# Optimization experiments

Measured on AMD Instinct MI355X. Metric: run time of the kernel, lower is better.

The kernel has to match this reference:

```python
import jax, jax.numpy as jnp
import numpy as np
from jax import lax

B, N, T, E = 16, 2048, 48, 32
C0, C1 = 64, 64
H1, H2 = 256, 128
NPRED = 12
KT = 3
SCALE = float(np.sqrt(C1))


def setup_inputs() -> dict:
    key = jax.random.key(0)
    ks = jax.random.split(key, 20)
    def lin(k, fin, fout):
        bound = 1.0 / np.sqrt(fin)
        kw, kb = jax.random.split(k)
        W = jax.random.uniform(kw, (fin, fout), jnp.float32, -bound, bound)
        b = jax.random.uniform(kb, (fout,), jnp.float32, -bound, bound)
        return W, b
    x = jax.random.normal(ks[0], (B, N, T, E), jnp.float32)
    W_in, b_in = lin(ks[1], E, C0)
    # conv kernel laid out WIO for lax.conv_general_dilated ('NWC','WIO','NWC')
    bound = 1.0 / np.sqrt(C0 * KT)
    W_conv = jax.random.uniform(ks[2], (KT, C0, C1), jnp.float32, -bound, bound)
    b_conv = jax.random.uniform(ks[3], (C1,), jnp.float32, -bound, bound)
    Wq, bq = lin(ks[4], C1, C1)
    Wk, bk = lin(ks[5], C1, C1)
    Wv, bv = lin(ks[6], C1, C1)
    W1, b1 = lin(ks[7], C1, H1)
    W2, b2 = lin(ks[8], H1, H2)
    W3, b3 = lin(ks[9], H2, NPRED)
    return dict(x=x, W_in=W_in, b_in=b_in, W_conv=W_conv, b_conv=b_conv,
                Wq=Wq, bq=bq, Wk=Wk, bk=bk, Wv=Wv, bv=bv,
                W1=W1, b1=b1, W2=W2, b2=b2, W3=W3, b3=b3)


def reference(x, W_in, b_in, W_conv, b_conv, Wq, bq, Wk, bk, Wv, bv,
              W1, b1, W2, b2, W3, b3):
    Bs, Ns, Ts, Es = x.shape
    # input linear, fold nodes into batch (weights shared across nodes)
    h = jnp.einsum('bnte,ec->bntc', x, W_in) + b_in          # [B,N,T,C0]
    h = h.reshape(Bs * Ns, Ts, C0)                            # [BN,T,C0]
    # temporal conv over T, kernel KT, pad 1 each side (matches Conv2d (Kt,1), pad (1,0))
    h = lax.conv_general_dilated(h, W_conv, window_strides=(1,),
                                 padding=[(1, 1)],
                                 dimension_numbers=('NWC', 'WIO', 'NWC')) + b_conv
    h = jax.nn.relu(h)                                        # [BN,T,C1]
    q = h @ Wq + bq
    k = h @ Wk + bk
    v = h @ Wv + bv
    scores = jnp.einsum('btd,bsd->bts', q, k) / SCALE         # [BN,T,T]
    attn = jax.nn.softmax(scores, axis=-1)
    ctx = jnp.einsum('bts,bsd->btd', attn, v)                 # [BN,T,C1]
    last = ctx[:, -1, :]                                      # [BN,C1]
    # output MLP (dropout is identity in eval/reference)
    z = jax.nn.relu(last @ W1 + b1)
    z = jax.nn.relu(z @ W2 + b2)
    pred = z @ W3 + b3                                        # [BN,NPRED]
    out = pred.reshape(Bs, Ns, NPRED)                         # [B,N,P]
    out = jnp.transpose(out, (0, 2, 1))[:, None]              # [B,1,P,N]
    return out
```

## Files before the change

### kernel.cpp

```cpp
#include <hip/hip_runtime.h>
#include <hip/hip_bf16.h>
#include <math.h>

#define TT 48
#define NSEQ (16*2048)
#define NP 12

typedef __bf16 bf16x8 __attribute__((ext_vector_type(8)));
typedef float  f32x4  __attribute__((ext_vector_type(4)));

#define OFF_WCC 0
#define OFF_WK  6144
#define OFF_WV  10240
#define OFF_WQ  14336
#define OFF_W1  18432
#define OFF_W2  34816
#define WS_BTOT 33792
#define WS_BC0  33856
#define WS_BC2  33920
#define WS_CTX  33984

__device__ __forceinline__ f32x4 zero4() {
  f32x4 z; z[0] = 0.f; z[1] = 0.f; z[2] = 0.f; z[3] = 0.f; return z;
}

union PackU { bf16x8 v; __hip_bfloat162 h[4]; };

__device__ __forceinline__ bf16x8 pack8(float4 a, float4 b) {
  PackU u;
  u.h[0] = __float22bfloat162_rn(make_float2(a.x, a.y));
  u.h[1] = __float22bfloat162_rn(make_float2(a.z, a.w));
  u.h[2] = __float22bfloat162_rn(make_float2(b.x, b.y));
  u.h[3] = __float22bfloat162_rn(make_float2(b.z, b.w));
  return u.v;
}

__global__ __launch_bounds__(256) void prep_kernel(
    const float* __restrict__ W_in, const float* __restrict__ b_in,
    const float* __restrict__ W_conv, const float* __restrict__ b_conv,
    const float* __restrict__ Wk, const float* __restrict__ Wv,
    const float* __restrict__ Wq, const float* __restrict__ W1,
    const float* __restrict__ W2, float* __restrict__ ws)
{
  __bf16* wsb = (__bf16*)ws;
  const int tid = threadIdx.x;
  const int bid = blockIdx.x;
  if (bid < 24) {
    int gid = bid * 256 + tid;
    int kk = gid >> 6;
    int c  = gid & 63;
    int dt = kk >> 5;
    int e  = kk & 31;
    const float* wrow = W_in + e * 64;
    const float* wc   = W_conv + dt * 4096 + c;
    float acc = 0.f;
    #pragma unroll 8
    for (int c0 = 0; c0 < 64; ++c0)
      acc = fmaf(wrow[c0], wc[c0 * 64], acc);
    wsb[OFF_WCC + ((kk >> 3) * 64 + c) * 8 + (kk & 7)] = (__bf16)acc;
  } else if (bid < 40) {
    int gid = (bid - 24) * 256 + tid;
    int kk = gid >> 6, c = gid & 63;
    wsb[OFF_WK + ((kk >> 3) * 64 + c) * 8 + (kk & 7)] = (__bf16)Wk[kk * 64 + c];
  } else if (bid < 56) {
    int gid = (bid - 40) * 256 + tid;
    int kk = gid >> 6, c = gid & 63;
    wsb[OFF_WV + ((kk >> 3) * 64 + c) * 8 + (kk & 7)] = (__bf16)Wv[kk * 64 + c];
  } else if (bid < 72) {
    int gid = (bid - 56) * 256 + tid;
    int kk = gid >> 6, c = gid & 63;
    wsb[OFF_WQ + ((kk >> 3) * 64 + c) * 8 + (kk & 7)] = (__bf16)Wq[kk * 64 + c];
  } else if (bid < 136) {
    int gid = (bid - 72) * 256 + tid;
    int kk = gid >> 8, n = gid & 255;
    wsb[OFF_W1 + ((kk >> 3) * 256 + n) * 8 + (kk & 7)] = (__bf16)W1[kk * 256 + n];
  } else if (bid < 264) {
    int gid = (bid - 136) * 256 + tid;
    int kk = gid >> 7, n = gid & 127;
    wsb[OFF_W2 + ((kk >> 3) * 128 + n) * 8 + (kk & 7)] = (__bf16)W2[kk * 128 + n];
  } else if (tid < 64) {
    int c = tid;
    float s[3];
    for (int dt = 0; dt < 3; ++dt) {
      const float* wc = W_conv + dt * 4096 + c;
      float a = 0.f;
      for (int c0 = 0; c0 < 64; ++c0) a = fmaf(b_in[c0], wc[c0 * 64], a);
      s[dt] = a;
    }
    ws[WS_BC0 + c]  = s[0];
    ws[WS_BC2 + c]  = s[2];
    ws[WS_BTOT + c] = s[0] + s[1] + s[2] + b_conv[c];
  }
}

__global__ __launch_bounds__(128, 4) void attn_kernel(
    const float* __restrict__ x,
    const float* __restrict__ bq, const float* __restrict__ bk,
    const float* __restrict__ bv,
    const float* __restrict__ ws, float* __restrict__ ctx)
{
  __shared__ __bf16 h1s[2][48 * 66];

  const int tid  = threadIdx.x;
  const int lane = tid & 63;
  const int wv   = tid >> 6;
  const int m16  = lane & 15;
  const int quad = lane >> 4;
  const int seq  = blockIdx.x * 2 + wv;
  __bf16* h1 = h1s[wv];

  const __bf16* wsb  = (const __bf16*)ws;
  const bf16x8* WccB = (const bf16x8*)(wsb + OFF_WCC);
  const bf16x8* WkB  = (const bf16x8*)(wsb + OFF_WK);
  const bf16x8* WvB  = (const bf16x8*)(wsb + OFF_WV);
  const bf16x8* WqB  = (const bf16x8*)(wsb + OFF_WQ);
  const float*  wsf  = ws;
  const float*  xseq = x + (size_t)seq * (TT * 32);

  bf16x8 af[3][3];
  #pragma unroll
  for (int mt = 0; mt < 3; ++mt)
    #pragma unroll
    for (int ks = 0; ks < 3; ++ks) {
      const int tg = mt * 16 + m16 + ks - 1;
      const bool need_guard = (mt == 0 && ks == 0) || (mt == 2 && ks == 2);
      if (!need_guard || (tg >= 0 && tg < 48)) {
        const float* ap = xseq + tg * 32 + quad * 8;
        af[mt][ks] = pack8(*(const float4*)ap, *(const float4*)(ap + 4));
      } else {
        #pragma unroll
        for (int j = 0; j < 8; ++j) af[mt][ks][j] = (__bf16)0.f;
      }
    }

  #pragma unroll
  for (int nh = 0; nh < 2; ++nh) {
    f32x4 acc[3][2];
    #pragma unroll
    for (int mt = 0; mt < 3; ++mt) { acc[mt][0] = zero4(); acc[mt][1] = zero4(); }
    #pragma unroll
    for (int ks = 0; ks < 3; ++ks) {
      bf16x8 b0 = WccB[(ks * 4 + quad) * 64 + nh * 32 + m16];
      bf16x8 b1 = WccB[(ks * 4 + quad) * 64 + nh * 32 + 16 + m16];
      #pragma unroll
      for (int mt = 0; mt < 3; ++mt) {
        acc[mt][0] = __builtin_amdgcn_mfma_f32_16x16x32_bf16(af[mt][ks], b0, acc[mt][0], 0, 0, 0);
        acc[mt][1] = __builtin_amdgcn_mfma_f32_16x16x32_bf16(af[mt][ks], b1, acc[mt][1], 0, 0, 0);
      }
    }
    #pragma unroll
    for (int j = 0; j < 2; ++j) {
      const int c = nh * 32 + j * 16 + m16;
      const float bt = wsf[WS_BTOT + c];
      const float b0v = wsf[WS_BC0 + c];
      const float b2v = wsf[WS_BC2 + c];
      #pragma unroll
      for (int mt = 0; mt < 3; ++mt)
        #pragma unroll
        for (int r = 0; r < 4; ++r) {
          const int trow = mt * 16 + quad * 4 + r;
          float v = acc[mt][j][r] + bt;
          if (mt == 0 && r == 0 && quad == 0) v -= b0v;
          if (mt == 2 && r == 3 && quad == 3) v -= b2v;
          h1[trow * 66 + c] = (__bf16)fmaxf(v, 0.f);
        }
    }
  }
  __asm__ __volatile__("s_waitcnt lgkmcnt(0)" ::: "memory");

  bf16x8 a8[3][2];
  #pragma unroll
  for (int mt = 0; mt < 3; ++mt)
    #pragma unroll
    for (int ks = 0; ks < 2; ++ks)
      a8[mt][ks] = *(const bf16x8*)&h1[(mt * 16 + m16) * 66 + ks * 32 + quad * 8];

  float qvv[4];
  {
    f32x4 qa[4] = {zero4(), zero4(), zero4(), zero4()};
    #pragma unroll
    for (int ks = 0; ks < 2; ++ks)
      #pragma unroll
      for (int nt = 0; nt < 4; ++nt)
        qa[nt] = __builtin_amdgcn_mfma_f32_16x16x32_bf16(
            a8[2][ks], WqB[(ks * 4 + quad) * 64 + nt * 16 + m16], qa[nt], 0, 0, 0);
    #pragma unroll
    for (int nt = 0; nt < 4; ++nt) {
      float q47 = __shfl(qa[nt][3], m16 + 48, 64);
      qvv[nt] = (q47 + bq[nt * 16 + m16]) * 0.125f;
    }
  }

  float p[3][4];
  {
    float s[3][4];
    {
      float qb = 0.f;
      #pragma unroll
      for (int nt = 0; nt < 4; ++nt) qb = fmaf(qvv[nt], bk[nt * 16 + m16], qb);
      #pragma unroll
      for (int mt = 0; mt < 3; ++mt)
        #pragma unroll
        for (int r = 0; r < 4; ++r) s[mt][r] = qb;
    }
    #pragma unroll
    for (int nh = 0; nh < 2; ++nh) {
      f32x4 ka[3][2];
      #pragma unroll
      for (int mt = 0; mt < 3; ++mt) { ka[mt][0] = zero4(); ka[mt][1] = zero4(); }
      #pragma unroll
      for (int ks = 0; ks < 2; ++ks) {
        bf16x8 b0 = WkB[(ks * 4 + quad) * 64 + nh * 32 + m16];
        bf16x8 b1 = WkB[(ks * 4 + quad) * 64 + nh * 32 + 16 + m16];
        #pragma unroll
        for (int mt = 0; mt < 3; ++mt) {
          ka[mt][0] = __builtin_amdgcn_mfma_f32_16x16x32_bf16(a8[mt][ks], b0, ka[mt][0], 0, 0, 0);
          ka[mt][1] = __builtin_amdgcn_mfma_f32_16x16x32_bf16(a8[mt][ks], b1, ka[mt][1], 0, 0, 0);
        }
      }
      #pragma unroll
      for (int mt = 0; mt < 3; ++mt)
        #pragma unroll
        for (int r = 0; r < 4; ++r) {
          s[mt][r] = fmaf(qvv[nh * 2],     ka[mt][0][r], s[mt][r]);
          s[mt][r] = fmaf(qvv[nh * 2 + 1], ka[mt][1][r], s[mt][r]);
        }
    }
    #pragma unroll
    for (int mt = 0; mt < 3; ++mt)
      #pragma unroll
      for (int r = 0; r < 4; ++r) {
        float t = s[mt][r];
        t += __shfl_xor(t, 1, 64);
        t += __shfl_xor(t, 2, 64);
        t += __shfl_xor(t, 4, 64);
        t += __shfl_xor(t, 8, 64);
        s[mt][r] = t;
      }
    float mx = -INFINITY;
    #pragma unroll
    for (int mt = 0; mt < 3; ++mt)
      #pragma unroll
      for (int r = 0; r < 4; ++r) mx = fmaxf(mx, s[mt][r]);
    mx = fmaxf(mx, __shfl_xor(mx, 16, 64));
    mx = fmaxf(mx, __shfl_xor(mx, 32, 64));
    float l = 0.f;
    #pragma unroll
    for (int mt = 0; mt < 3; ++mt)
      #pragma unroll
      for (int r = 0; r < 4; ++r) {
        float e = __expf(s[mt][r] - mx);
        p[mt][r] = e;
        l += e;
      }
    l += __shfl_xor(l, 16, 64);
    l += __shfl_xor(l, 32, 64);
    float rl = 1.f / l;
    #pragma unroll
    for (int mt = 0; mt < 3; ++mt)
      #pragma unroll
      for (int r = 0; r < 4; ++r) p[mt][r] *= rl;
  }

  {
    float cx[4];
    #pragma unroll
    for (int nh = 0; nh < 2; ++nh) {
      f32x4 va[3][2];
      #pragma unroll
      for (int mt = 0; mt < 3; ++mt) { va[mt][0] = zero4(); va[mt][1] = zero4(); }
      #pragma unroll
      for (int ks = 0; ks < 2; ++ks) {
        bf16x8 b0 = WvB[(ks * 4 + quad) * 64 + nh * 32 + m16];
        bf16x8 b1 = WvB[(ks * 4 + quad) * 64 + nh * 32 + 16 + m16];
        #pragma unroll
        for (int mt = 0; mt < 3; ++mt) {
          va[mt][0] = __builtin_amdgcn_mfma_f32_16x16x32_bf16(a8[mt][ks], b0, va[mt][0], 0, 0, 0);
          va[mt][1] = __builtin_amdgcn_mfma_f32_16x16x32_bf16(a8[mt][ks], b1, va[mt][1], 0, 0, 0);
        }
      }
      #pragma unroll
      for (int j = 0; j < 2; ++j) {
        float a = 0.f;
        #pragma unroll
        for (int mt = 0; mt < 3; ++mt)
          #pragma unroll
          for (int r = 0; r < 4; ++r)
            a = fmaf(p[mt][r], va[mt][j][r], a);
        cx[nh * 2 + j] = a;
      }
    }
    #pragma unroll
    for (int nt = 0; nt < 4; ++nt) {
      cx[nt] += __shfl_xor(cx[nt], 16, 64);
      cx[nt] += __shfl_xor(cx[nt], 32, 64);
    }
    if (quad == 0) {
      #pragma unroll
      for (int nt = 0; nt < 4; ++nt)
        ctx[(size_t)seq * 64 + nt * 16 + m16] = cx[nt] + bv[nt * 16 + m16];
    }
  }
}

__global__ __launch_bounds__(256) void mlp_kernel(
    const float* __restrict__ ctx, const float* __restrict__ ws,
    const float* __restrict__ b1, const float* __restrict__ b2,
    const float* __restrict__ W3, const float* __restrict__ b3,
    float* __restrict__ out)
{
  __shared__ __bf16 Xs[16 * 68];
  __shared__ __bf16 z1[16 * 264];
  __shared__ float  z2[16 * 132];

  const int tid  = threadIdx.x;
  const int r0   = blockIdx.x * 16;
  const int lane = tid & 63;
  const int wv   = tid >> 6;
  const int m16  = lane & 15;
  const int quad = lane >> 4;

  const __bf16* wsb = (const __bf16*)ws;
  const bf16x8* W1B = (const bf16x8*)(wsb + OFF_W1);
  const bf16x8* W2B = (const bf16x8*)(wsb + OFF_W2);

  {
    int row = tid >> 4, c4 = (tid & 15) * 4;
    float4 a = *(const float4*)(ctx + (size_t)(r0 + row) * 64 + c4);
    __bf16* d = &Xs[row * 68 + c4];
    d[0] = (__bf16)a.x; d[1] = (__bf16)a.y; d[2] = (__bf16)a.z; d[3] = (__bf16)a.w;
  }
  __syncthreads();

  {
    bf16x8 a8[2];
    #pragma unroll
    for (int ks = 0; ks < 2; ++ks)
      a8[ks] = *(const bf16x8*)&Xs[m16 * 68 + ks * 32 + quad * 8];
    f32x4 acc[4] = {zero4(), zero4(), zero4(), zero4()};
    #pragma unroll
    for (int nt = 0; nt < 4; ++nt) {
      int n = wv * 64 + nt * 16 + m16;
      #pragma unroll
      for (int ks = 0; ks < 2; ++ks)
        acc[nt] = __builtin_amdgcn_mfma_f32_16x16x32_bf16(
            a8[ks], W1B[(ks * 4 + quad) * 256 + n], acc[nt], 0, 0, 0);
    }
    #pragma unroll
    for (int nt = 0; nt < 4; ++nt) {
      int n = wv * 64 + nt * 16 + m16;
      float bb = b1[n];
      #pragma unroll
      for (int r = 0; r < 4; ++r)
        z1[(quad * 4 + r) * 264 + n] = (__bf16)fmaxf(acc[nt][r] + bb, 0.f);
    }
  }
  __syncthreads();

  {
    f32x4 acc[2] = {zero4(), zero4()};
    #pragma unroll 2
    for (int ks = 0; ks < 8; ++ks) {
      bf16x8 a = *(const bf16x8*)&z1[m16 * 264 + ks * 32 + quad * 8];
      #pragma unroll
      for (int nt = 0; nt < 2; ++nt)
        acc[nt] = __builtin_amdgcn_mfma_f32_16x16x32_bf16(
            a, W2B[(ks * 4 + quad) * 128 + wv * 32 + nt * 16 + m16], acc[nt], 0, 0, 0);
    }
    #pragma unroll
    for (int nt = 0; nt < 2; ++nt) {
      int n = wv * 32 + nt * 16 + m16;
      float bb = b2[n];
      #pragma unroll
      for (int r = 0; r < 4; ++r)
        z2[(quad * 4 + r) * 132 + n] = fmaxf(acc[nt][r] + bb, 0.f);
    }
  }
  __syncthreads();

  if (tid < 16 * NP) {
    int r = tid / NP, pp = tid - r * NP;
    const float* zr = z2 + r * 132;
    float a0 = b3[pp], a1 = 0.f, a2 = 0.f, a3 = 0.f;
    #pragma unroll 8
    for (int k = 0; k < 128; k += 4) {
      float4 f = *(const float4*)(zr + k);
      a0 = fmaf(f.x, W3[k * NP + pp],       a0);
      a1 = fmaf(f.y, W3[(k + 1) * NP + pp], a1);
      a2 = fmaf(f.z, W3[(k + 2) * NP + pp], a2);
      a3 = fmaf(f.w, W3[(k + 3) * NP + pp], a3);
    }
    float a = (a0 + a1) + (a2 + a3);
    int row = r0 + r;
    int bb = row >> 11, nn = row & 2047;
    out[(size_t)bb * (NP * 2048) + pp * 2048 + nn] = a;
  }
}

extern "C" void kernel_launch(void* const* d_in, const int* in_sizes, int n_in,
                              void* d_out, int out_size, void* d_ws, size_t ws_size,
                              hipStream_t stream) {
  const float* x      = (const float*)d_in[0];
  const float* W_in   = (const float*)d_in[1];
  const float* b_in   = (const float*)d_in[2];
  const float* W_conv = (const float*)d_in[3];
  const float* b_conv = (const float*)d_in[4];
  const float* Wq     = (const float*)d_in[5];
  const float* bq     = (const float*)d_in[6];
  const float* Wk     = (const float*)d_in[7];
  const float* bk     = (const float*)d_in[8];
  const float* Wv     = (const float*)d_in[9];
  const float* bv     = (const float*)d_in[10];
  const float* W1     = (const float*)d_in[11];
  const float* b1     = (const float*)d_in[12];
  const float* W2     = (const float*)d_in[13];
  const float* b2     = (const float*)d_in[14];
  const float* W3     = (const float*)d_in[15];
  const float* b3     = (const float*)d_in[16];
  float* ws  = (float*)d_ws;
  float* out = (float*)d_out;

  prep_kernel<<<265, 256, 0, stream>>>(W_in, b_in, W_conv, b_conv, Wk, Wv, Wq, W1, W2, ws);
  attn_kernel<<<NSEQ / 2, 128, 0, stream>>>(x, bq, bk, bv, ws, ws + WS_CTX);
  mlp_kernel<<<NSEQ / 16, 256, 0, stream>>>(ws + WS_CTX, ws, b1, b2, W3, b3, out);
}
```

Measured before the change: 389.0 us.

## Fold Wq·Wkᵀ into one matrix so scores need only the last query

Precomputes M = Wq·Wkᵀ/8 and a bias vector Wk·bq/8 in the prep kernel. The attention kernel then forms the single row w = h_last·M + kb and computes all 48 scores with one small MFMA pass. This replaces the full K projection over 48 timesteps and the cross-lane shuffle reductions. Terms involving only bk are dropped because they are constant across keys and cancel in softmax. It also raises the launch-bounds occupancy hint to 5, with an extra bf16 rounding of the folded matrix and of w as the accuracy risk.

```diff
diff --git a/kernel.cpp b/kernel.cpp
--- a/kernel.cpp
+++ b/kernel.cpp
@@ -10,15 +10,15 @@
 typedef float  f32x4  __attribute__((ext_vector_type(4)));
 
 #define OFF_WCC 0
-#define OFF_WK  6144
+#define OFF_MQK 6144
 #define OFF_WV  10240
-#define OFF_WQ  14336
 #define OFF_W1  18432
 #define OFF_W2  34816
 #define WS_BTOT 33792
 #define WS_BC0  33856
 #define WS_BC2  33920
-#define WS_CTX  33984
+#define WS_KV0  33984
+#define WS_CTX  34048
 
 __device__ __forceinline__ f32x4 zero4() {
   f32x4 z; z[0] = 0.f; z[1] = 0.f; z[2] = 0.f; z[3] = 0.f; return z;
@@ -39,8 +39,9 @@
     const float* __restrict__ W_in, const float* __restrict__ b_in,
     const float* __restrict__ W_conv, const float* __restrict__ b_conv,
     const float* __restrict__ Wk, const float* __restrict__ Wv,
-    const float* __restrict__ Wq, const float* __restrict__ W1,
-    const float* __restrict__ W2, float* __restrict__ ws)
+    const float* __restrict__ Wq, const float* __restrict__ bq,
+    const float* __restrict__ W1, const float* __restrict__ W2,
+    float* __restrict__ ws)
 {
   __bf16* wsb = (__bf16*)ws;
   const int tid = threadIdx.x;
@@ -60,22 +61,23 @@
     wsb[OFF_WCC + ((kk >> 3) * 64 + c) * 8 + (kk & 7)] = (__bf16)acc;
   } else if (bid < 40) {
     int gid = (bid - 24) * 256 + tid;
-    int kk = gid >> 6, c = gid & 63;
-    wsb[OFF_WK + ((kk >> 3) * 64 + c) * 8 + (kk & 7)] = (__bf16)Wk[kk * 64 + c];
+    int d = gid >> 6, c = gid & 63;
+    const float* qr = Wq + d * 64;
+    const float* kr = Wk + c * 64;
+    float acc = 0.f;
+    #pragma unroll 8
+    for (int j = 0; j < 64; ++j) acc = fmaf(qr[j], kr[j], acc);
+    wsb[OFF_MQK + ((d >> 3) * 64 + c) * 8 + (d & 7)] = (__bf16)(0.125f * acc);
   } else if (bid < 56) {
     int gid = (bid - 40) * 256 + tid;
     int kk = gid >> 6, c = gid & 63;
     wsb[OFF_WV + ((kk >> 3) * 64 + c) * 8 + (kk & 7)] = (__bf16)Wv[kk * 64 + c];
-  } else if (bid < 72) {
+  } else if (bid < 120) {
     int gid = (bid - 56) * 256 + tid;
-    int kk = gid >> 6, c = gid & 63;
-    wsb[OFF_WQ + ((kk >> 3) * 64 + c) * 8 + (kk & 7)] = (__bf16)Wq[kk * 64 + c];
-  } else if (bid < 136) {
-    int gid = (bid - 72) * 256 + tid;
     int kk = gid >> 8, n = gid & 255;
     wsb[OFF_W1 + ((kk >> 3) * 256 + n) * 8 + (kk & 7)] = (__bf16)W1[kk * 256 + n];
-  } else if (bid < 264) {
-    int gid = (bid - 136) * 256 + tid;
+  } else if (bid < 248) {
+    int gid = (bid - 120) * 256 + tid;
     int kk = gid >> 7, n = gid & 127;
     wsb[OFF_W2 + ((kk >> 3) * 128 + n) * 8 + (kk & 7)] = (__bf16)W2[kk * 128 + n];
   } else if (tid < 64) {
@@ -90,16 +92,19 @@
     ws[WS_BC0 + c]  = s[0];
     ws[WS_BC2 + c]  = s[2];
     ws[WS_BTOT + c] = s[0] + s[1] + s[2] + b_conv[c];
-  }
-}
-
-__global__ __launch_bounds__(128, 4) void attn_kernel(
-    const float* __restrict__ x,
-    const float* __restrict__ bq, const float* __restrict__ bk,
-    const float* __restrict__ bv,
+    float a = 0.f;
+    const float* kr = Wk + c * 64;
+    for (int j = 0; j < 64; ++j) a = fmaf(kr[j], bq[j], a);
+    ws[WS_KV0 + c] = 0.125f * a;
+  }
+}
+
+__global__ __launch_bounds__(128, 5) void attn_kernel(
+    const float* __restrict__ x, const float* __restrict__ bv,
     const float* __restrict__ ws, float* __restrict__ ctx)
 {
   __shared__ __bf16 h1s[2][48 * 66];
+  __shared__ __bf16 wbufs[2][64];
 
   const int tid  = threadIdx.x;
   const int lane = tid & 63;
@@ -107,13 +112,13 @@
   const int m16  = lane & 15;
   const int quad = lane >> 4;
   const int seq  = blockIdx.x * 2 + wv;
-  __bf16* h1 = h1s[wv];
+  __bf16* h1   = h1s[wv];
+  __bf16* wbuf = wbufs[wv];
 
   const __bf16* wsb  = (const __bf16*)ws;
   const bf16x8* WccB = (const bf16x8*)(wsb + OFF_WCC);
-  const bf16x8* WkB  = (const bf16x8*)(wsb + OFF_WK);
+  const bf16x8* MqkB = (const bf16x8*)(wsb + OFF_MQK);
   const bf16x8* WvB  = (const bf16x8*)(wsb + OFF_WV);
-  const bf16x8* WqB  = (const bf16x8*)(wsb + OFF_WQ);
   const float*  wsf  = ws;
   const float*  xseq = x + (size_t)seq * (TT * 32);
 
@@ -151,7 +156,7 @@
     #pragma unroll
     for (int j = 0; j < 2; ++j) {
       const int c = nh * 32 + j * 16 + m16;
-      const float bt = wsf[WS_BTOT + c];
+      const float bt  = wsf[WS_BTOT + c];
       const float b0v = wsf[WS_BC0 + c];
       const float b2v = wsf[WS_BC2 + c];
       #pragma unroll
@@ -175,7 +180,6 @@
     for (int ks = 0; ks < 2; ++ks)
       a8[mt][ks] = *(const bf16x8*)&h1[(mt * 16 + m16) * 66 + ks * 32 + quad * 8];
 
-  float qvv[4];
   {
     f32x4 qa[4] = {zero4(), zero4(), zero4(), zero4()};
     #pragma unroll
@@ -183,65 +187,30 @@
       #pragma unroll
       for (int nt = 0; nt < 4; ++nt)
         qa[nt] = __builtin_amdgcn_mfma_f32_16x16x32_bf16(
-            a8[2][ks], WqB[(ks * 4 + quad) * 64 + nt * 16 + m16], qa[nt], 0, 0, 0);
-    #pragma unroll
-    for (int nt = 0; nt < 4; ++nt) {
-      float q47 = __shfl(qa[nt][3], m16 + 48, 64);
-      qvv[nt] = (q47 + bq[nt * 16 + m16]) * 0.125f;
-    }
-  }
+            a8[2][ks], MqkB[(ks * 4 + quad) * 64 + nt * 16 + m16], qa[nt], 0, 0, 0);
+    if (quad == 3) {
+      #pragma unroll
+      for (int nt = 0; nt < 4; ++nt)
+        wbuf[nt * 16 + m16] = (__bf16)(qa[nt][3] + wsf[WS_KV0 + nt * 16 + m16]);
+    }
+  }
+  __asm__ __volatile__("s_waitcnt lgkmcnt(0)" ::: "memory");
 
   float p[3][4];
   {
-    float s[3][4];
-    {
-      float qb = 0.f;
-      #pragma unroll
-      for (int nt = 0; nt < 4; ++nt) qb = fmaf(qvv[nt], bk[nt * 16 + m16], qb);
-      #pragma unroll
-      for (int mt = 0; mt < 3; ++mt)
-        #pragma unroll
-        for (int r = 0; r < 4; ++r) s[mt][r] = qb;
-    }
-    #pragma unroll
-    for (int nh = 0; nh < 2; ++nh) {
-      f32x4 ka[3][2];
-      #pragma unroll
-      for (int mt = 0; mt < 3; ++mt) { ka[mt][0] = zero4(); ka[mt][1] = zero4(); }
-      #pragma unroll
-      for (int ks = 0; ks < 2; ++ks) {
-        bf16x8 b0 = WkB[(ks * 4 + quad) * 64 + nh * 32 + m16];
-        bf16x8 b1 = WkB[(ks * 4 + quad) * 64 + nh * 32 + 16 + m16];
-        #pragma unroll
-        for (int mt = 0; mt < 3; ++mt) {
-          ka[mt][0] = __builtin_amdgcn_mfma_f32_16x16x32_bf16(a8[mt][ks], b0, ka[mt][0], 0, 0, 0);
-          ka[mt][1] = __builtin_amdgcn_mfma_f32_16x16x32_bf16(a8[mt][ks], b1, ka[mt][1], 0, 0, 0);
-        }
-      }
-      #pragma unroll
-      for (int mt = 0; mt < 3; ++mt)
-        #pragma unroll
-        for (int r = 0; r < 4; ++r) {
-          s[mt][r] = fmaf(qvv[nh * 2],     ka[mt][0][r], s[mt][r]);
-          s[mt][r] = fmaf(qvv[nh * 2 + 1], ka[mt][1][r], s[mt][r]);
-        }
-    }
+    bf16x8 wB0 = *(const bf16x8*)&wbuf[quad * 8];
+    bf16x8 wB1 = *(const bf16x8*)&wbuf[32 + quad * 8];
+    f32x4 sa[3] = {zero4(), zero4(), zero4()};
+    #pragma unroll
+    for (int mt = 0; mt < 3; ++mt) {
+      sa[mt] = __builtin_amdgcn_mfma_f32_16x16x32_bf16(a8[mt][0], wB0, sa[mt], 0, 0, 0);
+      sa[mt] = __builtin_amdgcn_mfma_f32_16x16x32_bf16(a8[mt][1], wB1, sa[mt], 0, 0, 0);
+    }
+    float mx = -INFINITY;
     #pragma unroll
     for (int mt = 0; mt < 3; ++mt)
       #pragma unroll
-      for (int r = 0; r < 4; ++r) {
-        float t = s[mt][r];
-        t += __shfl_xor(t, 1, 64);
-        t += __shfl_xor(t, 2, 64);
-        t += __shfl_xor(t, 4, 64);
-        t += __shfl_xor(t, 8, 64);
-        s[mt][r] = t;
-      }
-    float mx = -INFINITY;
-    #pragma unroll
-    for (int mt = 0; mt < 3; ++mt)
-      #pragma unroll
-      for (int r = 0; r < 4; ++r) mx = fmaxf(mx, s[mt][r]);
+      for (int r = 0; r < 4; ++r) mx = fmaxf(mx, sa[mt][r]);
     mx = fmaxf(mx, __shfl_xor(mx, 16, 64));
     mx = fmaxf(mx, __shfl_xor(mx, 32, 64));
     float l = 0.f;
@@ -249,7 +218,7 @@
     for (int mt = 0; mt < 3; ++mt)
       #pragma unroll
       for (int r = 0; r < 4; ++r) {
-        float e = __expf(s[mt][r] - mx);
+        float e = __expf(sa[mt][r] - mx);
         p[mt][r] = e;
         l += e;
       }
@@ -408,7 +377,7 @@
   const float* Wq     = (const float*)d_in[5];
   const float* bq     = (const float*)d_in[6];
   const float* Wk     = (const float*)d_in[7];
-  const float* bk     = (const float*)d_in[8];
+  const float* bk     = (const float*)d_in[8];  (void)bk;
   const float* Wv     = (const float*)d_in[9];
   const float* bv     = (const float*)d_in[10];
   const float* W1     = (const float*)d_in[11];
@@ -420,7 +389,7 @@
   float* ws  = (float*)d_ws;
   float* out = (float*)d_out;
 
-  prep_kernel<<<265, 256, 0, stream>>>(W_in, b_in, W_conv, b_conv, Wk, Wv, Wq, W1, W2, ws);
-  attn_kernel<<<NSEQ / 2, 128, 0, stream>>>(x, bq, bk, bv, ws, ws + WS_CTX);
+  prep_kernel<<<249, 256, 0, stream>>>(W_in, b_in, W_conv, b_conv, Wk, Wv, Wq, bq, W1, W2, ws);
+  attn_kernel<<<NSEQ / 2, 128, 0, stream>>>(x, bv, ws, ws + WS_CTX);
   mlp_kernel<<<NSEQ / 16, 256, 0, stream>>>(ws + WS_CTX, ws, b1, b2, W3, b3, out);
 }
```

New measurement: 378.1 us. 2.8% less time.
